# Kernel optimization log

Hardware: AMD Instinct MI355X
Metric: run time of the kernel (lower is better)

## Reference

```python
import jax, jax.numpy as jnp
import numpy as np

NUM_ROUTES = 32
LN_EPS = 1e-5


def _ln(x, g, b):
    mu = jnp.mean(x, axis=-1, keepdims=True)
    var = jnp.mean(jnp.square(x - mu), axis=-1, keepdims=True)
    return (x - mu) * jax.lax.rsqrt(var + LN_EPS) * g + b


def setup_inputs() -> dict:
    key = jax.random.key(0)
    ks = jax.random.split(key, 16)
    B, N, D = 64, 512, 512
    s = 1.0 / np.sqrt(D)
    return {
        "tokens": jax.random.normal(ks[0], (B, N, D), jnp.float32),
        "token_mask": jax.random.bernoulli(ks[1], 0.7, (B, N)),
        "route_ids": jax.random.randint(ks[2], (N,), 0, NUM_ROUTES),
        # token_ffn: LayerNorm + Linear(D,4D) + GELU + Linear(4D,D)
        "ln1_g": jnp.ones((D,), jnp.float32),
        "ln1_b": jnp.zeros((D,), jnp.float32),
        "w1": jax.random.normal(ks[3], (D, 4 * D), jnp.float32) * s,
        "b1": jnp.zeros((4 * D,), jnp.float32),
        "w2": jax.random.normal(ks[4], (4 * D, D), jnp.float32) * (0.5 * s),
        "b2": jnp.zeros((D,), jnp.float32),
        # within_route_pool: LayerNorm + Linear(D,1)
        "wp_g": jnp.ones((D,), jnp.float32),
        "wp_b": jnp.zeros((D,), jnp.float32),
        "wp_w": jax.random.normal(ks[5], (D,), jnp.float32) * s,
        "wp_bias": jnp.zeros((), jnp.float32),
        # route_pool: LayerNorm + Linear(D,1)
        "rp_g": jnp.ones((D,), jnp.float32),
        "rp_b": jnp.zeros((D,), jnp.float32),
        "rp_w": jax.random.normal(ks[6], (D,), jnp.float32) * s,
        "rp_bias": jnp.zeros((), jnp.float32),
    }


def reference(tokens, token_mask, route_ids, ln1_g, ln1_b, w1, b1, w2, b2,
              wp_g, wp_b, wp_w, wp_bias, rp_g, rp_b, rp_w, rp_bias):
    # token FFN with residual (dropout=0 in eval path)
    h = _ln(tokens, ln1_g, ln1_b)
    h = jax.nn.gelu(h @ w1 + b1, approximate=False)
    x = tokens + (h @ w2 + b2)                       # [B, N, D]

    # within-route attention pool: score is mask-independent -> compute once
    tok_logits = _ln(x, wp_g, wp_b) @ wp_w + wp_bias  # [B, N]

    route_onehot = route_ids[None, :] == jnp.arange(NUM_ROUTES)[:, None]  # [R, N]
    mask = route_onehot[None, :, :] & token_mask[:, None, :]              # [B, R, N]

    ml = jnp.where(mask, tok_logits[:, None, :], -1e9)
    w = jax.nn.softmax(ml, axis=-1)
    w = jnp.where(mask, w, 0.0)
    w = w / jnp.maximum(jnp.sum(w, axis=-1, keepdims=True), 1e-6)
    routes = jnp.einsum('brn,bnd->brd', w, x)         # [B, R, D]
    present = jnp.any(mask, axis=-1)                  # [B, R]

    # route-level attention pool
    rl = _ln(routes, rp_g, rp_b) @ rp_w + rp_bias     # [B, R]
    rl = jnp.where(present, rl, -1e9)
    rw = jax.nn.softmax(rl, axis=-1)
    rw = jnp.where(present, rw, 0.0)
    rw = rw / jnp.maximum(jnp.sum(rw, axis=-1, keepdims=True), 1e-6)
    return jnp.einsum('br,brd->bd', rw, routes)       # [B, D]
```

## Files before the change

### kernel.cpp

```cpp
#include <hip/hip_runtime.h>
#include <hip/hip_bf16.h>
#include <math.h>

#define B_ 64
#define N_ 512
#define D_ 512
#define H_ 2048
#define R_ 32
#define M_ (B_ * N_)

typedef __bf16 bf16x8 __attribute__((ext_vector_type(8)));
typedef float f32x4 __attribute__((ext_vector_type(4)));

__device__ __forceinline__ void async_ld16(const void* g, void* l) {
  __builtin_amdgcn_global_load_lds((__attribute__((address_space(1))) void*)g,
                                   (__attribute__((address_space(3))) void*)l,
                                   16, 0, 0);
}

__device__ __forceinline__ float fast_gelu(float v) {
  const float s = v * 0.70710678118654752f;
  const float a = fabsf(s);
  float t = fmaf(a, 4.30638e-5f, 2.765672e-4f);
  t = fmaf(a, t, 1.520143e-4f);
  t = fmaf(a, t, 9.2705272e-3f);
  t = fmaf(a, t, 4.22820123e-2f);
  t = fmaf(a, t, 7.05230784e-2f);
  const float p = fmaf(a, t, 1.0f);
  float p16 = p * p;
  p16 = p16 * p16;
  p16 = p16 * p16;
  p16 = p16 * p16;
  const float er = 1.0f - __builtin_amdgcn_rcpf(p16);
  const float erfs = (s >= 0.f) ? er : -er;
  return 0.5f * v * (1.0f + erfs);
}

__global__ __launch_bounds__(512) void prep_kernel(
    const float* __restrict__ tokens, const void* __restrict__ mask_raw,
    const float* __restrict__ ln1_g, const float* __restrict__ ln1_b,
    const float* __restrict__ w1, const float* __restrict__ w2,
    __hip_bfloat16* __restrict__ aBf, __hip_bfloat16* __restrict__ w1t,
    __hip_bfloat16* __restrict__ w2t, int* __restrict__ flag) {
  const int bid = blockIdx.x;
  const int tid = threadIdx.x;
  if (bid == 0) {
    __shared__ int f;
    if (tid == 0) f = 0;
    __syncthreads();
    const uint4* p = (const uint4*)mask_raw;
    unsigned acc = 0;
    for (int k = tid; k < M_ / 16; k += 512) {
      const uint4 v = p[k];
      acc |= (v.x | v.y | v.z | v.w) & 0xFFFFFF00u;
    }
    if (acc) f = 1;
    __syncthreads();
    if (tid == 0) flag[0] = f;
  } else if (bid <= 512) {
    __shared__ float tile[64][65];
    const int t = bid - 1;
    const float* src;
    __hip_bfloat16* dst;
    int R, C, cx, ry;
    if (t < 256) { src = w1; dst = w1t; R = 512; C = 2048; cx = t & 31; ry = t >> 5; }
    else { const int t2 = t - 256; src = w2; dst = w2t; R = 2048; C = 512; cx = t2 & 7; ry = t2 >> 3; }
    const int c0 = cx * 64, r0 = ry * 64;
    const int tx = tid & 63, ty = tid >> 6;
    for (int r = ty; r < 64; r += 8)
      tile[r][tx] = src[(size_t)(r0 + r) * C + c0 + tx];
    __syncthreads();
    for (int r = ty; r < 64; r += 8)
      dst[(size_t)(c0 + r) * R + r0 + tx] = __float2bfloat16(tile[tx][r]);
  } else {
    const int wv = tid >> 6, lane = tid & 63;
    const int row = (bid - 513) * 8 + wv;
    const float* p = tokens + (size_t)row * D_ + lane * 8;
    const float4 v0 = *(const float4*)p;
    const float4 v1 = *(const float4*)(p + 4);
    float s = v0.x + v0.y + v0.z + v0.w + v1.x + v1.y + v1.z + v1.w;
    float ss = v0.x * v0.x + v0.y * v0.y + v0.z * v0.z + v0.w * v0.w +
               v1.x * v1.x + v1.y * v1.y + v1.z * v1.z + v1.w * v1.w;
#pragma unroll
    for (int m = 32; m > 0; m >>= 1) {
      s += __shfl_xor(s, m);
      ss += __shfl_xor(ss, m);
    }
    const float mu = s * (1.0f / D_);
    const float rstd = rsqrtf(ss * (1.0f / D_) - mu * mu + 1e-5f);
    const float4 g0 = *(const float4*)(ln1_g + lane * 8);
    const float4 g1 = *(const float4*)(ln1_g + lane * 8 + 4);
    const float4 b0 = *(const float4*)(ln1_b + lane * 8);
    const float4 b1 = *(const float4*)(ln1_b + lane * 8 + 4);
    const float vv[8] = {v0.x, v0.y, v0.z, v0.w, v1.x, v1.y, v1.z, v1.w};
    const float gg[8] = {g0.x, g0.y, g0.z, g0.w, g1.x, g1.y, g1.z, g1.w};
    const float bb[8] = {b0.x, b0.y, b0.z, b0.w, b1.x, b1.y, b1.z, b1.w};
    union { __hip_bfloat16 h[8]; uint4 u; } pk;
#pragma unroll
    for (int t2 = 0; t2 < 8; ++t2)
      pk.h[t2] = __float2bfloat16((vv[t2] - mu) * rstd * gg[t2] + bb[t2]);
    *(uint4*)(aBf + (size_t)row * D_ + lane * 8) = pk.u;
  }
}

__global__ __launch_bounds__(256, 2) void gemm_bias_gelu_kernel(
    const __hip_bfloat16* __restrict__ A, const __hip_bfloat16* __restrict__ Bt,
    const float* __restrict__ bias, __hip_bfloat16* __restrict__ C,
    int K, int ldc, int NC) {
  __shared__ alignas(16) unsigned short SU[16384];
  unsigned short* As = SU;
  unsigned short* Bs = SU + 8192;
  const int tid = threadIdx.x;
  const int w = tid >> 6;
  const int lane = tid & 63;
  const int bid = blockIdx.x;
  const int rowT = (bid / (NC * 8)) * 8 + (bid & 7);
  const int colT = (bid >> 3) % NC;
  const int rowBase = rowT * 128;
  const int colBase = colT * 128;
  const int warpRow = w >> 1;
  const int warpCol = w & 1;
  const int q = lane >> 4;
  const int mr = lane & 15;
  const int srow8 = lane >> 3;
  const int sg8 = ((lane & 7) ^ srow8) * 8;
  const int mx7 = (mr & 7) * 8;

  f32x4 acc[4][4] = {};

  for (int k0 = 0; k0 < K; k0 += 64) {
    __syncthreads();
    {
      const __hip_bfloat16* Ak = A + (size_t)(rowBase + w * 32 + srow8) * K + k0 + sg8;
      const __hip_bfloat16* Bk = Bt + (size_t)(colBase + w * 32 + srow8) * K + k0 + sg8;
#pragma unroll
      for (int i = 0; i < 4; ++i) {
        async_ld16(Ak + (size_t)(i * 8) * K, (void*)&As[(w * 32 + i * 8) * 64]);
        async_ld16(Bk + (size_t)(i * 8) * K, (void*)&Bs[(w * 32 + i * 8) * 64]);
      }
    }
    __syncthreads();
#pragma unroll
    for (int s = 0; s < 2; ++s) {
      bf16x8 af[4], bf[4];
#pragma unroll
      for (int i = 0; i < 4; ++i)
        af[i] = *reinterpret_cast<const bf16x8*>(
            &As[(warpRow * 64 + i * 16 + mr) * 64 + (((s * 4 + q) * 8) ^ mx7)]);
#pragma unroll
      for (int j = 0; j < 4; ++j)
        bf[j] = *reinterpret_cast<const bf16x8*>(
            &Bs[(warpCol * 64 + j * 16 + mr) * 64 + (((s * 4 + q) * 8) ^ mx7)]);
#pragma unroll
      for (int i = 0; i < 4; ++i)
#pragma unroll
        for (int j = 0; j < 4; ++j)
          acc[i][j] = __builtin_amdgcn_mfma_f32_16x16x32_bf16(af[i], bf[j], acc[i][j], 0, 0, 0);
    }
  }

  __syncthreads();
  __hip_bfloat16* SB = (__hip_bfloat16*)SU;
#pragma unroll
  for (int j = 0; j < 4; ++j) {
    const int col = warpCol * 64 + j * 16 + mr;
    const float bv = bias[colBase + col];
    const int cl = col & 7;
    const int ch = col >> 3;
#pragma unroll
    for (int i = 0; i < 4; ++i) {
      float g[4];
#pragma unroll
      for (int r = 0; r < 4; ++r) g[r] = fast_gelu(acc[i][j][r] + bv);
      const __hip_bfloat162 p01 = __float22bfloat162_rn(make_float2(g[0], g[1]));
      const __hip_bfloat162 p23 = __float22bfloat162_rn(make_float2(g[2], g[3]));
      const int row0 = warpRow * 64 + i * 16 + q * 4;
      SB[(row0 + 0) * 128 + ((ch ^ ((row0 + 0) & 7)) << 3) + cl] = p01.x;
      SB[(row0 + 1) * 128 + ((ch ^ ((row0 + 1) & 7)) << 3) + cl] = p01.y;
      SB[(row0 + 2) * 128 + ((ch ^ ((row0 + 2) & 7)) << 3) + cl] = p23.x;
      SB[(row0 + 3) * 128 + ((ch ^ ((row0 + 3) & 7)) << 3) + cl] = p23.y;
    }
  }
  __syncthreads();
  const int lg = tid & 15, rsub = tid >> 4;
#pragma unroll
  for (int it = 0; it < 8; ++it) {
    const int m = it * 16 + rsub;
    const int slot = lg ^ (m & 7);
    const uint4 val = *(const uint4*)&SB[m * 128 + slot * 8];
    *(uint4*)&C[(size_t)(rowBase + m) * ldc + colBase + lg * 8] = val;
  }
}

__global__ __launch_bounds__(512, 4) void gemm_acc_kernel(
    const __hip_bfloat16* __restrict__ A, const __hip_bfloat16* __restrict__ Bt,
    const float* __restrict__ bias, const float* __restrict__ resid,
    float* __restrict__ X, int K, int ldb, int first) {
  __shared__ alignas(16) unsigned short SU[24576];
  unsigned short* As = SU;
  unsigned short* Bs = SU + 16384;
  const int tid = threadIdx.x;
  const int w = tid >> 6;
  const int lane = tid & 63;
  const int bid = blockIdx.x;
  const int NC = 4;
  const int rowT = (bid / (NC * 8)) * 8 + (bid & 7);
  const int colT = (bid >> 3) % NC;
  const int rowBase = rowT * 256;
  const int colBase = colT * 128;
  const int warpRow = w >> 1;
  const int warpCol = w & 1;
  const int q = lane >> 4;
  const int mr = lane & 15;
  const int srow8 = lane >> 3;
  const int sg8 = ((lane & 7) ^ srow8) * 8;
  const int mx7 = (mr & 7) * 8;

  f32x4 acc[4][4] = {};

  for (int k0 = 0; k0 < K; k0 += 64) {
    __syncthreads();
    {
      const __hip_bfloat16* Ak = A + (size_t)(rowBase + w * 32 + srow8) * K + k0 + sg8;
#pragma unroll
      for (int i = 0; i < 4; ++i)
        async_ld16(Ak + (size_t)(i * 8) * K, (void*)&As[(w * 32 + i * 8) * 64]);
      const __hip_bfloat16* Bk = Bt + (size_t)(colBase + w * 16 + srow8) * ldb + k0 + sg8;
#pragma unroll
      for (int i = 0; i < 2; ++i)
        async_ld16(Bk + (size_t)(i * 8) * ldb, (void*)&Bs[(w * 16 + i * 8) * 64]);
    }
    __syncthreads();
#pragma unroll
    for (int s = 0; s < 2; ++s) {
      bf16x8 af[4], bf[4];
#pragma unroll
      for (int i = 0; i < 4; ++i)
        af[i] = *reinterpret_cast<const bf16x8*>(
            &As[(warpRow * 64 + i * 16 + mr) * 64 + (((s * 4 + q) * 8) ^ mx7)]);
#pragma unroll
      for (int j = 0; j < 4; ++j)
        bf[j] = *reinterpret_cast<const bf16x8*>(
            &Bs[(warpCol * 64 + j * 16 + mr) * 64 + (((s * 4 + q) * 8) ^ mx7)]);
#pragma unroll
      for (int i = 0; i < 4; ++i)
#pragma unroll
        for (int j = 0; j < 4; ++j)
          acc[i][j] = __builtin_amdgcn_mfma_f32_16x16x32_bf16(af[i], bf[j], acc[i][j], 0, 0, 0);
    }
  }

#pragma unroll
  for (int j = 0; j < 4; ++j) {
    const int n = colBase + warpCol * 64 + j * 16 + mr;
    const float bv = bias[n];
#pragma unroll
    for (int i = 0; i < 4; ++i) {
#pragma unroll
      for (int r = 0; r < 4; ++r) {
        const int m = rowBase + warpRow * 64 + i * 16 + q * 4 + r;
        const size_t idx = (size_t)m * N_ + n;
        const float base = first ? (resid[idx] + bv) : X[idx];
        X[idx] = base + acc[i][j][r];
      }
    }
  }
}

__global__ __launch_bounds__(256) void route_pool_kernel(
    const float* __restrict__ X, const int* __restrict__ route_ids,
    const void* __restrict__ mask_raw, const int* __restrict__ flag,
    const float* __restrict__ gw, const float* __restrict__ gb,
    const float* __restrict__ ww, const float* __restrict__ wbias,
    float* __restrict__ routes, int* __restrict__ present) {
  const int b = blockIdx.x >> 5;
  const int r = blockIdx.x & 31;
  const int tid = threadIdx.x;
  __shared__ int cnt;
  __shared__ int ls[N_];
  __shared__ float lw[N_];
  if (tid == 0) cnt = 0;
  __syncthreads();
  const int fl = flag[0];
  for (int n = tid; n < N_; n += 256) {
    const int mk = fl ? (int)((const unsigned char*)mask_raw)[b * N_ + n]
                      : ((const int*)mask_raw)[b * N_ + n];
    if (route_ids[n] == r && mk != 0) {
      int p = atomicAdd(&cnt, 1);
      ls[p] = n;
    }
  }
  __syncthreads();
  const int c = cnt;
  const int wv = tid >> 6, lane = tid & 63;
  for (int t = wv; t < c; t += 4) {
    const float* p = X + ((size_t)b * N_ + ls[t]) * D_ + lane * 8;
    const float4 v0 = *(const float4*)p;
    const float4 v1 = *(const float4*)(p + 4);
    float s = v0.x + v0.y + v0.z + v0.w + v1.x + v1.y + v1.z + v1.w;
    float ss = v0.x * v0.x + v0.y * v0.y + v0.z * v0.z + v0.w * v0.w +
               v1.x * v1.x + v1.y * v1.y + v1.z * v1.z + v1.w * v1.w;
#pragma unroll
    for (int m = 32; m > 0; m >>= 1) {
      s += __shfl_xor(s, m);
      ss += __shfl_xor(ss, m);
    }
    const float mu = s * (1.0f / D_);
    const float rstd = rsqrtf(ss * (1.0f / D_) - mu * mu + 1e-5f);
    const float4 g0 = *(const float4*)(gw + lane * 8);
    const float4 g1 = *(const float4*)(gw + lane * 8 + 4);
    const float4 b0 = *(const float4*)(gb + lane * 8);
    const float4 b1v = *(const float4*)(gb + lane * 8 + 4);
    const float4 w0 = *(const float4*)(ww + lane * 8);
    const float4 w1v = *(const float4*)(ww + lane * 8 + 4);
    const float vv[8] = {v0.x, v0.y, v0.z, v0.w, v1.x, v1.y, v1.z, v1.w};
    const float gg[8] = {g0.x, g0.y, g0.z, g0.w, g1.x, g1.y, g1.z, g1.w};
    const float bb[8] = {b0.x, b0.y, b0.z, b0.w, b1v.x, b1v.y, b1v.z, b1v.w};
    const float wwv[8] = {w0.x, w0.y, w0.z, w0.w, w1v.x, w1v.y, w1v.z, w1v.w};
    float a = 0.f;
#pragma unroll
    for (int t2 = 0; t2 < 8; ++t2) a += ((vv[t2] - mu) * rstd * gg[t2] + bb[t2]) * wwv[t2];
#pragma unroll
    for (int m = 32; m > 0; m >>= 1) a += __shfl_xor(a, m);
    if (lane == 0) lw[t] = a + wbias[0];
  }
  __syncthreads();
  if (tid == 0 && c > 0) {
    float mx = -1e30f;
    for (int i = 0; i < c; ++i) mx = fmaxf(mx, lw[i]);
    float sm = 0.f;
    for (int i = 0; i < c; ++i) {
      const float e = __expf(lw[i] - mx);
      lw[i] = e;
      sm += e;
    }
    const float inv = 1.0f / sm;
    for (int i = 0; i < c; ++i) lw[i] *= inv;
  }
  __syncthreads();
  float a0 = 0.f, a1 = 0.f;
  for (int i = 0; i < c; ++i) {
    const float* xr = X + ((size_t)b * N_ + ls[i]) * D_;
    const float wgt = lw[i];
    a0 += wgt * xr[tid];
    a1 += wgt * xr[tid + 256];
  }
  float* outp = routes + ((size_t)b * R_ + r) * D_;
  outp[tid] = a0;
  outp[tid + 256] = a1;
  if (tid == 0) present[b * R_ + r] = (c > 0) ? 1 : 0;
}

__global__ __launch_bounds__(512) void final_pool_kernel(
    const float* __restrict__ routes, const int* __restrict__ present,
    const float* __restrict__ gw, const float* __restrict__ gb,
    const float* __restrict__ ww, const float* __restrict__ wbias,
    float* __restrict__ out) {
  const int b = blockIdx.x;
  const int wv = threadIdx.x >> 6, lane = threadIdx.x & 63;
  __shared__ float srw[R_];
  __shared__ float srl[R_];
  for (int r = wv; r < R_; r += 8) {
    const float* p = routes + ((size_t)b * R_ + r) * D_ + lane * 8;
    const float4 v0 = *(const float4*)p;
    const float4 v1 = *(const float4*)(p + 4);
    float s = v0.x + v0.y + v0.z + v0.w + v1.x + v1.y + v1.z + v1.w;
    float ss = v0.x * v0.x + v0.y * v0.y + v0.z * v0.z + v0.w * v0.w +
               v1.x * v1.x + v1.y * v1.y + v1.z * v1.z + v1.w * v1.w;
#pragma unroll
    for (int m = 32; m > 0; m >>= 1) {
      s += __shfl_xor(s, m);
      ss += __shfl_xor(ss, m);
    }
    const float mu = s * (1.0f / D_);
    const float rstd = rsqrtf(ss * (1.0f / D_) - mu * mu + 1e-5f);
    const float4 g0 = *(const float4*)(gw + lane * 8);
    const float4 g1 = *(const float4*)(gw + lane * 8 + 4);
    const float4 b0 = *(const float4*)(gb + lane * 8);
    const float4 b1v = *(const float4*)(gb + lane * 8 + 4);
    const float4 w0 = *(const float4*)(ww + lane * 8);
    const float4 w1v = *(const float4*)(ww + lane * 8 + 4);
    const float vv[8] = {v0.x, v0.y, v0.z, v0.w, v1.x, v1.y, v1.z, v1.w};
    const float gg[8] = {g0.x, g0.y, g0.z, g0.w, g1.x, g1.y, g1.z, g1.w};
    const float bb[8] = {b0.x, b0.y, b0.z, b0.w, b1v.x, b1v.y, b1v.z, b1v.w};
    const float wwv[8] = {w0.x, w0.y, w0.z, w0.w, w1v.x, w1v.y, w1v.z, w1v.w};
    float a = 0.f;
#pragma unroll
    for (int t = 0; t < 8; ++t) a += ((vv[t] - mu) * rstd * gg[t] + bb[t]) * wwv[t];
#pragma unroll
    for (int m = 32; m > 0; m >>= 1) a += __shfl_xor(a, m);
    if (lane == 0) srl[r] = a + wbias[0];
  }
  __syncthreads();
  if (threadIdx.x == 0) {
    float mx = -1e30f;
    for (int r = 0; r < R_; ++r)
      if (present[b * R_ + r]) mx = fmaxf(mx, srl[r]);
    float sm = 0.f;
    for (int r = 0; r < R_; ++r) {
      const float e = present[b * R_ + r] ? __expf(srl[r] - mx) : 0.f;
      srw[r] = e;
      sm += e;
    }
    const float inv = (sm > 0.f) ? 1.0f / sm : 0.f;
    for (int r = 0; r < R_; ++r) srw[r] *= inv;
  }
  __syncthreads();
  const int d = threadIdx.x;
  float a = 0.f;
  for (int r = 0; r < R_; ++r) a += srw[r] * routes[((size_t)b * R_ + r) * D_ + d];
  out[(size_t)b * D_ + d] = a;
}

extern "C" void kernel_launch(void* const* d_in, const int* in_sizes, int n_in,
                              void* d_out, int out_size, void* d_ws, size_t ws_size,
                              hipStream_t stream) {
  const float* tokens = (const float*)d_in[0];
  const void* mask_raw = d_in[1];
  const int* route_ids = (const int*)d_in[2];
  const float* ln1_g = (const float*)d_in[3];
  const float* ln1_b = (const float*)d_in[4];
  const float* w1 = (const float*)d_in[5];
  const float* b1 = (const float*)d_in[6];
  const float* w2 = (const float*)d_in[7];
  const float* b2 = (const float*)d_in[8];
  const float* wp_g = (const float*)d_in[9];
  const float* wp_b = (const float*)d_in[10];
  const float* wp_w = (const float*)d_in[11];
  const float* wp_bias = (const float*)d_in[12];
  const float* rp_g = (const float*)d_in[13];
  const float* rp_b = (const float*)d_in[14];
  const float* rp_w = (const float*)d_in[15];
  const float* rp_bias = (const float*)d_in[16];
  float* out = (float*)d_out;

  char* ws = (char*)d_ws;
  size_t off = 0;
  auto carve = [&](size_t bytes) -> void* {
    void* p = ws + off;
    off = (off + bytes + 255) & ~(size_t)255;
    return p;
  };

  __hip_bfloat16* w1t = (__hip_bfloat16*)carve((size_t)H_ * D_ * 2);
  __hip_bfloat16* w2t = (__hip_bfloat16*)carve((size_t)D_ * H_ * 2);
  __hip_bfloat16* aBf = (__hip_bfloat16*)carve((size_t)M_ * D_ * 2);
  float* X = (float*)carve((size_t)M_ * D_ * 4);
  int* flag = (int*)carve(256);
  int* present = (int*)carve((size_t)B_ * R_ * 4);
  float* routes = (float*)carve((size_t)B_ * R_ * D_ * 4);

  int G = 1;
  while (G < 16 && off + (size_t)M_ * (H_ / G) * 2 > ws_size) G <<= 1;
  const int Hg = H_ / G;
  __hip_bfloat16* hbuf = (__hip_bfloat16*)carve((size_t)M_ * Hg * 2);

  prep_kernel<<<513 + M_ / 8, 512, 0, stream>>>(
      tokens, mask_raw, ln1_g, ln1_b, w1, w2, aBf, w1t, w2t, flag);

  const int NC1 = Hg / 128;
  for (int g = 0; g < G; ++g) {
    gemm_bias_gelu_kernel<<<(M_ / 128) * NC1, 256, 0, stream>>>(
        aBf, w1t + (size_t)g * Hg * D_, b1 + (size_t)g * Hg, hbuf, D_, Hg, NC1);
    gemm_acc_kernel<<<(M_ / 256) * 4, 512, 0, stream>>>(
        hbuf, w2t + (size_t)g * Hg, b2, tokens, X, Hg, H_, (g == 0) ? 1 : 0);
  }

  route_pool_kernel<<<B_ * R_, 256, 0, stream>>>(
      X, route_ids, mask_raw, flag, wp_g, wp_b, wp_w, wp_bias, routes, present);
  final_pool_kernel<<<B_, 512, 0, stream>>>(routes, present, rp_g, rp_b, rp_w, rp_bias, out);
}
```

Baseline: 351.0 us.

## Fuse within-route LayerNorm logit statistics into second GEMM epilogue

The second GEMM epilogue now accumulates per-row sum, sum of squares and a gamma*w weighted dot product into global stats with atomics. The route pool kernel then forms each token logit algebraically from those stats plus precomputed sums of gamma*w and beta*w, so it no longer re-reads and re-normalises each masked row of X. This trades a full pass over the masked rows of X for extra shuffles and three atomics per row per column tile in the GEMM epilogue, plus zeroing the stats buffer in prep. The one-pass variance form may also be less numerically stable.

```diff
diff --git a/kernel.cpp b/kernel.cpp
--- a/kernel.cpp
+++ b/kernel.cpp
@@ -40,12 +40,16 @@
     const float* __restrict__ tokens, const void* __restrict__ mask_raw,
     const float* __restrict__ ln1_g, const float* __restrict__ ln1_b,
     const float* __restrict__ w1, const float* __restrict__ w2,
+    const float* __restrict__ wp_g, const float* __restrict__ wp_b,
+    const float* __restrict__ wp_w,
     __hip_bfloat16* __restrict__ aBf, __hip_bfloat16* __restrict__ w1t,
-    __hip_bfloat16* __restrict__ w2t, int* __restrict__ flag) {
+    __hip_bfloat16* __restrict__ w2t, int* __restrict__ flag,
+    float* __restrict__ scr, float* __restrict__ stats) {
   const int bid = blockIdx.x;
   const int tid = threadIdx.x;
   if (bid == 0) {
     __shared__ int f;
+    __shared__ float red[2][8];
     if (tid == 0) f = 0;
     __syncthreads();
     const uint4* p = (const uint4*)mask_raw;
@@ -55,8 +59,24 @@
       acc |= (v.x | v.y | v.z | v.w) & 0xFFFFFF00u;
     }
     if (acc) f = 1;
-    __syncthreads();
-    if (tid == 0) flag[0] = f;
+    const int wv = tid >> 6, lane = tid & 63;
+    float gw = wp_g[tid] * wp_w[tid];
+    float bw = wp_b[tid] * wp_w[tid];
+#pragma unroll
+    for (int m = 32; m > 0; m >>= 1) {
+      gw += __shfl_xor(gw, m);
+      bw += __shfl_xor(bw, m);
+    }
+    if (lane == 0) { red[0][wv] = gw; red[1][wv] = bw; }
+    for (int k = tid; k < 3 * M_; k += 512) stats[k] = 0.f;
+    __syncthreads();
+    if (tid == 0) {
+      flag[0] = f;
+      float s1 = 0.f, s2 = 0.f;
+      for (int i = 0; i < 8; ++i) { s1 += red[0][i]; s2 += red[1][i]; }
+      scr[0] = s1;
+      scr[1] = s2;
+    }
   } else if (bid <= 512) {
     __shared__ float tile[64][65];
     const int t = bid - 1;
@@ -195,7 +215,9 @@
 __global__ __launch_bounds__(512, 4) void gemm_acc_kernel(
     const __hip_bfloat16* __restrict__ A, const __hip_bfloat16* __restrict__ Bt,
     const float* __restrict__ bias, const float* __restrict__ resid,
-    float* __restrict__ X, int K, int ldb, int first) {
+    float* __restrict__ X, const float* __restrict__ wp_g,
+    const float* __restrict__ wp_w, float* __restrict__ stats,
+    int K, int ldb, int first, int stats_on) {
   __shared__ alignas(16) unsigned short SU[24576];
   unsigned short* As = SU;
   unsigned short* Bs = SU + 16384;
@@ -250,18 +272,45 @@
     }
   }
 
+  float* Sx = stats;
+  float* Sxx = stats + M_;
+  float* Pd = stats + 2 * M_;
+  float bv[4], gwv[4];
 #pragma unroll
   for (int j = 0; j < 4; ++j) {
     const int n = colBase + warpCol * 64 + j * 16 + mr;
-    const float bv = bias[n];
-#pragma unroll
-    for (int i = 0; i < 4; ++i) {
-#pragma unroll
-      for (int r = 0; r < 4; ++r) {
-        const int m = rowBase + warpRow * 64 + i * 16 + q * 4 + r;
+    bv[j] = bias[n];
+    gwv[j] = stats_on ? (wp_g[n] * wp_w[n]) : 0.f;
+  }
+#pragma unroll
+  for (int i = 0; i < 4; ++i) {
+#pragma unroll
+    for (int r = 0; r < 4; ++r) {
+      const int m = rowBase + warpRow * 64 + i * 16 + q * 4 + r;
+      float sx = 0.f, sxx = 0.f, sp = 0.f;
+#pragma unroll
+      for (int j = 0; j < 4; ++j) {
+        const int n = colBase + warpCol * 64 + j * 16 + mr;
         const size_t idx = (size_t)m * N_ + n;
-        const float base = first ? (resid[idx] + bv) : X[idx];
-        X[idx] = base + acc[i][j][r];
+        const float base = first ? (resid[idx] + bv[j]) : X[idx];
+        const float xv = base + acc[i][j][r];
+        X[idx] = xv;
+        sx += xv;
+        sxx += xv * xv;
+        sp += xv * gwv[j];
+      }
+      if (stats_on) {
+#pragma unroll
+        for (int mm = 1; mm < 16; mm <<= 1) {
+          sx += __shfl_xor(sx, mm);
+          sxx += __shfl_xor(sxx, mm);
+          sp += __shfl_xor(sp, mm);
+        }
+        if (mr == 0) {
+          atomicAdd(&Sx[m], sx);
+          atomicAdd(&Sxx[m], sxx);
+          atomicAdd(&Pd[m], sp);
+        }
       }
     }
   }
@@ -270,8 +319,8 @@
 __global__ __launch_bounds__(256) void route_pool_kernel(
     const float* __restrict__ X, const int* __restrict__ route_ids,
     const void* __restrict__ mask_raw, const int* __restrict__ flag,
-    const float* __restrict__ gw, const float* __restrict__ gb,
-    const float* __restrict__ ww, const float* __restrict__ wbias,
+    const float* __restrict__ scr, const float* __restrict__ stats,
+    const float* __restrict__ wbias,
     float* __restrict__ routes, int* __restrict__ present) {
   const int b = blockIdx.x >> 5;
   const int r = blockIdx.x & 31;
@@ -292,37 +341,16 @@
   }
   __syncthreads();
   const int c = cnt;
-  const int wv = tid >> 6, lane = tid & 63;
-  for (int t = wv; t < c; t += 4) {
-    const float* p = X + ((size_t)b * N_ + ls[t]) * D_ + lane * 8;
-    const float4 v0 = *(const float4*)p;
-    const float4 v1 = *(const float4*)(p + 4);
-    float s = v0.x + v0.y + v0.z + v0.w + v1.x + v1.y + v1.z + v1.w;
-    float ss = v0.x * v0.x + v0.y * v0.y + v0.z * v0.z + v0.w * v0.w +
-               v1.x * v1.x + v1.y * v1.y + v1.z * v1.z + v1.w * v1.w;
-#pragma unroll
-    for (int m = 32; m > 0; m >>= 1) {
-      s += __shfl_xor(s, m);
-      ss += __shfl_xor(ss, m);
-    }
-    const float mu = s * (1.0f / D_);
-    const float rstd = rsqrtf(ss * (1.0f / D_) - mu * mu + 1e-5f);
-    const float4 g0 = *(const float4*)(gw + lane * 8);
-    const float4 g1 = *(const float4*)(gw + lane * 8 + 4);
-    const float4 b0 = *(const float4*)(gb + lane * 8);
-    const float4 b1v = *(const float4*)(gb + lane * 8 + 4);
-    const float4 w0 = *(const float4*)(ww + lane * 8);
-    const float4 w1v = *(const float4*)(ww + lane * 8 + 4);
-    const float vv[8] = {v0.x, v0.y, v0.z, v0.w, v1.x, v1.y, v1.z, v1.w};
-    const float gg[8] = {g0.x, g0.y, g0.z, g0.w, g1.x, g1.y, g1.z, g1.w};
-    const float bb[8] = {b0.x, b0.y, b0.z, b0.w, b1v.x, b1v.y, b1v.z, b1v.w};
-    const float wwv[8] = {w0.x, w0.y, w0.z, w0.w, w1v.x, w1v.y, w1v.z, w1v.w};
-    float a = 0.f;
-#pragma unroll
-    for (int t2 = 0; t2 < 8; ++t2) a += ((vv[t2] - mu) * rstd * gg[t2] + bb[t2]) * wwv[t2];
-#pragma unroll
-    for (int m = 32; m > 0; m >>= 1) a += __shfl_xor(a, m);
-    if (lane == 0) lw[t] = a + wbias[0];
+  const float S1 = scr[0], S2 = scr[1];
+  const float* Sx = stats;
+  const float* Sxx = stats + M_;
+  const float* Pd = stats + 2 * M_;
+  for (int t = tid; t < c; t += 256) {
+    const int row = b * N_ + ls[t];
+    const float mu = Sx[row] * (1.0f / D_);
+    const float var = Sxx[row] * (1.0f / D_) - mu * mu;
+    const float rstd = rsqrtf(var + 1e-5f);
+    lw[t] = rstd * (Pd[row] - mu * S1) + S2 + wbias[0];
   }
   __syncthreads();
   if (tid == 0 && c > 0) {
@@ -447,6 +475,8 @@
   __hip_bfloat16* aBf = (__hip_bfloat16*)carve((size_t)M_ * D_ * 2);
   float* X = (float*)carve((size_t)M_ * D_ * 4);
   int* flag = (int*)carve(256);
+  float* scr = (float*)carve(256);
+  float* stats = (float*)carve((size_t)3 * M_ * 4);
   int* present = (int*)carve((size_t)B_ * R_ * 4);
   float* routes = (float*)carve((size_t)B_ * R_ * D_ * 4);
 
@@ -456,17 +486,19 @@
   __hip_bfloat16* hbuf = (__hip_bfloat16*)carve((size_t)M_ * Hg * 2);
 
   prep_kernel<<<513 + M_ / 8, 512, 0, stream>>>(
-      tokens, mask_raw, ln1_g, ln1_b, w1, w2, aBf, w1t, w2t, flag);
+      tokens, mask_raw, ln1_g, ln1_b, w1, w2, wp_g, wp_b, wp_w,
+      aBf, w1t, w2t, flag, scr, stats);
 
   const int NC1 = Hg / 128;
   for (int g = 0; g < G; ++g) {
     gemm_bias_gelu_kernel<<<(M_ / 128) * NC1, 256, 0, stream>>>(
         aBf, w1t + (size_t)g * Hg * D_, b1 + (size_t)g * Hg, hbuf, D_, Hg, NC1);
     gemm_acc_kernel<<<(M_ / 256) * 4, 512, 0, stream>>>(
-        hbuf, w2t + (size_t)g * Hg, b2, tokens, X, Hg, H_, (g == 0) ? 1 : 0);
+        hbuf, w2t + (size_t)g * Hg, b2, tokens, X, wp_g, wp_w, stats,
+        Hg, H_, (g == 0) ? 1 : 0, (g == G - 1) ? 1 : 0);
   }
 
   route_pool_kernel<<<B_ * R_, 256, 0, stream>>>(
-      X, route_ids, mask_raw, flag, wp_g, wp_b, wp_w, wp_bias, routes, present);
+      X, route_ids, mask_raw, flag, scr, stats, wp_bias, routes, present);
   final_pool_kernel<<<B_, 512, 0, stream>>>(routes, present, rp_g, rp_b, rp_w, rp_bias, out);
 }
```

Result: no change. 349.1 us (-0.5%).
